# Performance work log

Measured on AMD Instinct MI355X. Metric: run time of the kernel, lower is better.

## Reference

```python
import jax, jax.numpy as jnp
import numpy as np

N, K, FEAT = 64, 32, 1024      # nodes, neighbors per node, input feature dim
C1, F1 = 4, 16                 # layer1: out_channels=4, out_features=hidden[0]/4=16
C2, F2 = 32, 1                 # layer2: out_channels=hidden[1]=32, out_features=1
NUM_CLASS = 10
BN_EPS = 1e-5


def _sgnroot(x):
    return jnp.sign(x) * jnp.sqrt(jnp.clip(jnp.abs(x), 1e-8))


def _feature_adjacency(x, nb):
    # x: (N,c,f), nb: (N,K,c,f) -> adj: (N,c,f,f)
    fadj = jnp.einsum('nca,nkcb->ncab', x, nb)          # sum over K neighbors
    fadj = fadj + jnp.swapaxes(fadj, -2, -1)
    s = _sgnroot(fadj)
    out = s / (jnp.abs(s).sum(axis=1, keepdims=True) + 1e-7)  # row-normalize over channel dim
    return jnp.where(jnp.isnan(out), 0.0, out)


def _layer(x, nb, W, c_out, f_out):
    # FeatTrans1d.forward: adjacency build + batched matmul + full-width conv (== dense contraction)
    n = x.shape[0]
    adj = _feature_adjacency(x, nb)                     # (N,c,f,f)
    xa = jnp.einsum('ncab,ncb->nca', adj, x)            # adj @ x
    x2 = jnp.einsum('ocf,ncf->no', W, xa).reshape(n, c_out, f_out)
    na = jnp.einsum('ncab,nkcb->nkca', adj, nb)         # per-node adj applied to its neighbors
    nb2 = jnp.einsum('ocf,nkcf->nko', W, na).reshape(n, -1, c_out, f_out)
    return x2, nb2


def _bn_softsign_x(x, w, b):
    # BatchNorm1d (training stats over batch+feature dims) + Softsign; x: (N,C,F)
    m = x.mean(axis=(0, 2), keepdims=True)
    v = x.var(axis=(0, 2), keepdims=True)
    y = (x - m) / jnp.sqrt(v + BN_EPS) * w[None, :, None] + b[None, :, None]
    return y / (1.0 + jnp.abs(y))


def _bn_softsign_nb(x, w, b):
    # each node's neighbor set is normalized independently (list comprehension in original); x: (N,K,C,F)
    m = x.mean(axis=(1, 3), keepdims=True)
    v = x.var(axis=(1, 3), keepdims=True)
    y = (x - m) / jnp.sqrt(v + BN_EPS) * w[None, None, :, None] + b[None, None, :, None]
    return y / (1.0 + jnp.abs(y))


def setup_inputs() -> dict:
    key = jax.random.key(0)
    ks = jax.random.split(key, 6)
    return {
        'x': jax.random.normal(ks[0], (N, 1, FEAT), jnp.float32),
        'neighbor': jax.random.normal(ks[1], (N, K, 1, FEAT), jnp.float32),
        'W1': jax.random.normal(ks[2], (C1 * F1, 1, FEAT), jnp.float32) * (1.0 / FEAT) ** 0.5,
        'W2': jax.random.normal(ks[3], (C2 * F2, C1, F1), jnp.float32) * (1.0 / (C1 * F1)) ** 0.5,
        'bn1_w': jnp.ones((C1,), jnp.float32),
        'bn1_b': jnp.zeros((C1,), jnp.float32),
        'bn2_w': jnp.ones((C2,), jnp.float32),
        'bn2_b': jnp.zeros((C2,), jnp.float32),
        'lin_w': jax.random.normal(ks[4], (NUM_CLASS, C2 * F2), jnp.float32) * (1.0 / (C2 * F2)) ** 0.5,
        'lin_b': jnp.zeros((NUM_CLASS,), jnp.float32),
    }


def reference(x, neighbor, W1, W2, bn1_w, bn1_b, bn2_w, bn2_b, lin_w, lin_b):
    x1, nb1 = _layer(x, neighbor, W1, C1, F1)           # (N,4,16), (N,K,4,16)
    x1 = _bn_softsign_x(x1, bn1_w, bn1_b)
    nb1 = _bn_softsign_nb(nb1, bn1_w, bn1_b)
    x2, _ = _layer(x1, nb1, W2, C2, F2)                 # (N,32,1)
    x2 = _bn_softsign_x(x2, bn2_w, bn2_b)
    return x2.reshape(x2.shape[0], -1) @ lin_w.T + lin_b  # (N,NUM_CLASS)
```

## Files before the change

kernel.cpp:

```cpp
#include <hip/hip_runtime.h>

typedef unsigned short u16;
typedef short short8 __attribute__((ext_vector_type(8)));
typedef float floatx4 __attribute__((ext_vector_type(4)));
typedef float floatx2 __attribute__((ext_vector_type(2)));
typedef unsigned int uintx4 __attribute__((ext_vector_type(4)));
typedef unsigned int uintx2 __attribute__((ext_vector_type(2)));
typedef u16 ushortx4 __attribute__((ext_vector_type(4)));

#define FEAT 1024
#define KNB  32

__device__ __forceinline__ u16 f2bf(float f) {
    unsigned u = __float_as_uint(f);
    u += 0x7fffu + ((u >> 16) & 1u);
    return (u16)(u >> 16);
}
__device__ __forceinline__ unsigned pack2bf(float a, float b) {
    return (unsigned)f2bf(a) | ((unsigned)f2bf(b) << 16);
}
__device__ __forceinline__ float softsign(float v) { return v / (1.f + fabsf(v)); }

union Frag { uintx4 q; unsigned d[4]; short8 v; };

__global__ __launch_bounds__(256, 2) void k2_main(
    const float* __restrict__ xg, const float* __restrict__ nbg,
    const float* __restrict__ w1g, float* __restrict__ pws)
{
    __shared__ float sS[FEAT];
    __shared__ float sX[FEAT];
    __shared__ u16  sY[34 * 1024];

    const int t = threadIdx.x;
    const int n = blockIdx.x >> 3;
    const int chunk = blockIdx.x & 7;
    const int chunkbase = chunk * 128;
    const int w = t >> 6;
    const int l = t & 63;
    const int m = l & 15;
    const int g = l >> 4;

    {
        ushortx4 z4 = {0, 0, 0, 0};
        *(ushortx4*)&sY[33 * 1024 + t * 4] = z4;
    }
    {
        floatx4 xv = *(const floatx4*)(xg + (size_t)n * FEAT + t * 4);
        *(floatx4*)&sX[t * 4] = xv;
        ushortx4 xb4 = {f2bf(xv[0]), f2bf(xv[1]), f2bf(xv[2]), f2bf(xv[3])};
        *(ushortx4*)&sY[t * 4] = xb4;
    }
    {
        const float* nbase = nbg + ((size_t)n * KNB) * FEAT + t * 4;
        floatx4 sacc = {0.f, 0.f, 0.f, 0.f};
        #pragma unroll 4
        for (int k = 0; k < KNB; ++k) {
            floatx4 v = *(const floatx4*)(nbase + (size_t)k * FEAT);
            sacc += v;
            int row = k + 1;
            int c16 = (t >> 1) ^ (row & 7);
            ushortx4 p4 = {f2bf(v[0]), f2bf(v[1]), f2bf(v[2]), f2bf(v[3])};
            *(ushortx4*)&sY[row * 1024 + c16 * 8 + (t & 1) * 4] = p4;
        }
        *(floatx4*)&sS[t * 4] = sacc;
    }

    const float xa0 = xg[(size_t)n * FEAT + chunkbase + w * 32 + m];
    const float xa1 = xg[(size_t)n * FEAT + chunkbase + w * 32 + 16 + m];
    __syncthreads();
    const float Sa0 = sS[chunkbase + w * 32 + m];
    const float Sa1 = sS[chunkbase + w * 32 + 16 + m];

    const u16* b2base = (m == 0) ? &sY[32 * 1024] : &sY[33 * 1024];
    const int sw = (m & 7);

    floatx4 acc[2][3];
    #pragma unroll
    for (int i = 0; i < 2; ++i)
        #pragma unroll
        for (int j = 0; j < 3; ++j) { floatx4 z = {0.f, 0.f, 0.f, 0.f}; acc[i][j] = z; }

    const floatx2 vxa0 = {xa0, xa0}, vxa1 = {xa1, xa1};
    const floatx2 vSa0 = {Sa0, Sa0}, vSa1 = {Sa1, Sa1};

    #pragma unroll 2
    for (int s = 0; s < 32; ++s) {
        const int bloc = s * 32 + g * 8;
        const int cidx = bloc >> 3;

        floatx4 xq0 = *(const floatx4*)&sX[bloc];
        floatx4 xq1 = *(const floatx4*)&sX[bloc + 4];
        floatx4 sq0 = *(const floatx4*)&sS[bloc];
        floatx4 sq1 = *(const floatx4*)&sS[bloc + 4];

        Frag af0, af1;
        #pragma unroll
        for (int p = 0; p < 4; ++p) {
            floatx2 xbp = (p < 2) ? ((p == 0) ? (floatx2){xq0[0], xq0[1]} : (floatx2){xq0[2], xq0[3]})
                                  : ((p == 2) ? (floatx2){xq1[0], xq1[1]} : (floatx2){xq1[2], xq1[3]});
            floatx2 sbp = (p < 2) ? ((p == 0) ? (floatx2){sq0[0], sq0[1]} : (floatx2){sq0[2], sq0[3]})
                                  : ((p == 2) ? (floatx2){sq1[0], sq1[1]} : (floatx2){sq1[2], sq1[3]});
            floatx2 u0 = xbp * vSa0 + sbp * vxa0;
            floatx2 u1 = xbp * vSa1 + sbp * vxa1;
            uintx2 b0b = __builtin_bit_cast(uintx2, u0);
            uintx2 b1b = __builtin_bit_cast(uintx2, u1);
            af0.d[p] = 0x3F803F80u | (b0b.y & 0x80000000u) | ((b0b.x >> 16) & 0x8000u);
            af1.d[p] = 0x3F803F80u | (b1b.y & 0x80000000u) | ((b1b.x >> 16) & 0x8000u);
        }

        Frag b0, b1, b2;
        b0.q = *(const uintx4*)&sY[ m       * 1024 + ((cidx ^ sw) << 3)];
        b1.q = *(const uintx4*)&sY[(16 + m) * 1024 + ((cidx ^ sw) << 3)];
        b2.q = *(const uintx4*)&b2base[cidx << 3];

        acc[0][0] = __builtin_amdgcn_mfma_f32_16x16x32_bf16(af0.v, b0.v, acc[0][0], 0, 0, 0);
        acc[0][1] = __builtin_amdgcn_mfma_f32_16x16x32_bf16(af0.v, b1.v, acc[0][1], 0, 0, 0);
        acc[0][2] = __builtin_amdgcn_mfma_f32_16x16x32_bf16(af0.v, b2.v, acc[0][2], 0, 0, 0);
        acc[1][0] = __builtin_amdgcn_mfma_f32_16x16x32_bf16(af1.v, b0.v, acc[1][0], 0, 0, 0);
        acc[1][1] = __builtin_amdgcn_mfma_f32_16x16x32_bf16(af1.v, b1.v, acc[1][1], 0, 0, 0);
        acc[1][2] = __builtin_amdgcn_mfma_f32_16x16x32_bf16(af1.v, b2.v, acc[1][2], 0, 0, 0);
    }
    __syncthreads();

    u16* sZ = sY;
    #pragma unroll
    for (int ti = 0; ti < 2; ++ti)
        #pragma unroll
        for (int jt = 0; jt < 3; ++jt) {
            int j = jt * 16 + m;
            int aloc = w * 32 + ti * 16 + g * 4;
            ushortx4 zz;
            zz.x = f2bf(acc[ti][jt][0]);
            zz.y = f2bf(acc[ti][jt][1]);
            zz.z = f2bf(acc[ti][jt][2]);
            zz.w = f2bf(acc[ti][jt][3]);
            *(ushortx4*)&sZ[j * 136 + aloc] = zz;
        }
    __syncthreads();

    floatx4 a2[3];
    #pragma unroll
    for (int j = 0; j < 3; ++j) { floatx4 z = {0.f, 0.f, 0.f, 0.f}; a2[j] = z; }
    #pragma unroll
    for (int kc = 0; kc < 4; ++kc) {
        const float* wsrc = w1g + (size_t)(w * 16 + m) * FEAT + chunkbase + kc * 32 + g * 8;
        floatx4 wf0 = *(const floatx4*)wsrc;
        floatx4 wf1 = *(const floatx4*)(wsrc + 4);
        Frag wb;
        wb.d[0] = pack2bf(wf0[0], wf0[1]);
        wb.d[1] = pack2bf(wf0[2], wf0[3]);
        wb.d[2] = pack2bf(wf1[0], wf1[1]);
        wb.d[3] = pack2bf(wf1[2], wf1[3]);
        #pragma unroll
        for (int jt = 0; jt < 3; ++jt) {
            Frag za;
            za.q = *(const uintx4*)&sZ[(jt * 16 + m) * 136 + kc * 32 + g * 8];
            a2[jt] = __builtin_amdgcn_mfma_f32_16x16x32_bf16(za.v, wb.v, a2[jt], 0, 0, 0);
        }
    }
    float* pbase = pws + (size_t)(n * 8 + chunk) * 33 * 64;
    #pragma unroll
    for (int jt = 0; jt < 3; ++jt)
        #pragma unroll
        for (int r = 0; r < 4; ++r) {
            int j = jt * 16 + g * 4 + r;
            if (j < 33) pbase[j * 64 + w * 16 + m] = a2[jt][r];
        }
}

__global__ __launch_bounds__(256, 1) void kB(
    const float* __restrict__ pws, const float* __restrict__ bn1w,
    const float* __restrict__ bn1b, const float* __restrict__ w2g,
    float* __restrict__ x22ws)
{
    __shared__ float sx2[64 * 64];
    __shared__ float snb[32 * 64];
    __shared__ float sx1[64], sS1[64], sadj[4 * 16 * 16], sxa[64];
    __shared__ float ssc[4], sbi[4], ssc2[4], sbi2[4];
    const int t = threadIdx.x;
    const int n = blockIdx.x;

    #pragma unroll
    for (int r = 0; r < 4; ++r) {
        int slot = t + r * 256;
        int nn = slot >> 4, oc = slot & 15;
        const float* p = pws + (size_t)nn * 16896 + oc * 4;
        floatx4 tmp[8];
        #pragma unroll
        for (int c = 0; c < 8; ++c) tmp[c] = *(const floatx4*)(p + c * 2112);
        floatx4 s01 = tmp[0] + tmp[1], s23 = tmp[2] + tmp[3];
        floatx4 s45 = tmp[4] + tmp[5], s67 = tmp[6] + tmp[7];
        *(floatx4*)&sx2[slot * 4] = (s01 + s23) + (s45 + s67);
    }
    #pragma unroll
    for (int r = 0; r < 2; ++r) {
        int slot = t + r * 256;
        int k = slot >> 4, oc = slot & 15;
        const float* p = pws + (size_t)n * 16896 + (1 + k) * 64 + oc * 4;
        floatx4 tmp[8];
        #pragma unroll
        for (int c = 0; c < 8; ++c) tmp[c] = *(const floatx4*)(p + c * 2112);
        floatx4 s01 = tmp[0] + tmp[1], s23 = tmp[2] + tmp[3];
        floatx4 s45 = tmp[4] + tmp[5], s67 = tmp[6] + tmp[7];
        *(floatx4*)&snb[slot * 4] = (s01 + s23) + (s45 + s67);
    }
    __syncthreads();
    {
        int cc = t >> 6, l2 = t & 63;
        float s = 0.f, s2 = 0.f;
        #pragma unroll
        for (int i = 0; i < 16; ++i) {
            int idx = l2 * 16 + i;
            int nn = idx >> 4, f = idx & 15;
            float v = sx2[nn * 64 + cc * 16 + f];
            s += v; s2 += v * v;
        }
        float s3 = 0.f, s4 = 0.f;
        #pragma unroll
        for (int i = 0; i < 8; ++i) {
            int idx = l2 * 8 + i;
            int k = idx >> 4, f = idx & 15;
            float v = snb[k * 64 + cc * 16 + f];
            s3 += v; s4 += v * v;
        }
        #pragma unroll
        for (int off = 32; off > 0; off >>= 1) {
            s  += __shfl_down(s, off);  s2 += __shfl_down(s2, off);
            s3 += __shfl_down(s3, off); s4 += __shfl_down(s4, off);
        }
        if (l2 == 0) {
            float wv = bn1w[cc], bv = bn1b[cc];
            float mean = s * (1.f / 1024.f);
            float var = s2 * (1.f / 1024.f) - mean * mean;
            float rs = rsqrtf(var + 1e-5f);
            ssc[cc] = rs * wv;
            sbi[cc] = bv - mean * rs * wv;
            float mean2 = s3 * (1.f / 512.f);
            float var2 = s4 * (1.f / 512.f) - mean2 * mean2;
            float rs2 = rsqrtf(var2 + 1e-5f);
            ssc2[cc] = rs2 * wv;
            sbi2[cc] = bv - mean2 * rs2 * wv;
        }
    }
    __syncthreads();
    if (t < 64) {
        int cc = t >> 4;
        sx1[t] = softsign(sx2[n * 64 + t] * ssc[cc] + sbi[cc]);
        float a = 0.f;
        for (int k = 0; k < KNB; ++k)
            a += softsign(snb[k * 64 + t] * ssc2[cc] + sbi2[cc]);
        sS1[t] = a;
    }
    __syncthreads();
    {
        int a = t >> 4, b = t & 15;
        float sc[4]; float den = 1e-7f;
        #pragma unroll
        for (int c = 0; c < 4; ++c) {
            float u = sx1[c * 16 + a] * sS1[c * 16 + b] + sx1[c * 16 + b] * sS1[c * 16 + a];
            float r = sqrtf(fmaxf(fabsf(u), 1e-8f));
            sc[c] = copysignf(r, u);
            den += r;
        }
        float inv = 1.f / den;
        #pragma unroll
        for (int c = 0; c < 4; ++c) sadj[(c * 16 + a) * 16 + b] = sc[c] * inv;
    }
    __syncthreads();
    if (t < 64) {
        int cc = t >> 4;
        float a = 0.f;
        #pragma unroll
        for (int b = 0; b < 16; ++b) a += sadj[t * 16 + b] * sx1[cc * 16 + b];
        sxa[t] = a;
    }
    __syncthreads();
    if (t < 32) {
        float a = 0.f;
        #pragma unroll
        for (int cf = 0; cf < 64; ++cf) a += w2g[t * 64 + cf] * sxa[cf];
        x22ws[n * 32 + t] = a;
    }
}

__global__ __launch_bounds__(256) void kC(
    const float* __restrict__ x22ws, const float* __restrict__ bn2w,
    const float* __restrict__ bn2b, const float* __restrict__ linw,
    const float* __restrict__ linb, float* __restrict__ outg)
{
    __shared__ float sy[64 * 32];
    __shared__ float ssc[32], sbi[32];
    __shared__ float sx[64 * 32];
    const int t = threadIdx.x;
    #pragma unroll
    for (int r = 0; r < 8; ++r) sx[t + r * 256] = x22ws[t + r * 256];
    __syncthreads();
    if (t < 32) {
        float s = 0.f, s2 = 0.f;
        for (int nn = 0; nn < 64; ++nn) {
            float v = sx[nn * 32 + t];
            s += v; s2 += v * v;
        }
        float mean = s * (1.f / 64.f);
        float var = s2 * (1.f / 64.f) - mean * mean;
        float rs = rsqrtf(var + 1e-5f);
        float wv = bn2w[t], bv = bn2b[t];
        ssc[t] = rs * wv;
        sbi[t] = bv - mean * rs * wv;
    }
    __syncthreads();
    #pragma unroll
    for (int r = 0; r < 8; ++r) {
        int idx = t + r * 256;
        int o = idx & 31;
        sy[idx] = softsign(sx[idx] * ssc[o] + sbi[o]);
    }
    __syncthreads();
    for (int r = 0; r < 3; ++r) {
        int idx = t + r * 256;
        if (idx < 640) {
            int nn = idx / 10, cls = idx % 10;
            float a = linb[cls];
            #pragma unroll
            for (int o = 0; o < 32; ++o) a += sy[nn * 32 + o] * linw[cls * 32 + o];
            outg[idx] = a;
        }
    }
}

extern "C" void kernel_launch(void* const* d_in, const int* in_sizes, int n_in,
                              void* d_out, int out_size, void* d_ws, size_t ws_size,
                              hipStream_t stream) {
    (void)in_sizes; (void)n_in; (void)out_size; (void)ws_size;
    const float* xg   = (const float*)d_in[0];
    const float* nbg  = (const float*)d_in[1];
    const float* w1g  = (const float*)d_in[2];
    const float* w2g  = (const float*)d_in[3];
    const float* bn1w = (const float*)d_in[4];
    const float* bn1b = (const float*)d_in[5];
    const float* bn2w = (const float*)d_in[6];
    const float* bn2b = (const float*)d_in[7];
    const float* linw = (const float*)d_in[8];
    const float* linb = (const float*)d_in[9];

    float* pws   = (float*)d_ws;
    float* x22ws = pws + (size_t)64 * 8 * 33 * 64;
    float* outg  = (float*)d_out;

    k2_main<<<dim3(512), dim3(256), 0, stream>>>(xg, nbg, w1g, pws);
    kB<<<dim3(64), dim3(256), 0, stream>>>(pws, bn1w, bn1b, w2g, x22ws);
    kC<<<dim3(1), dim3(256), 0, stream>>>(x22ws, bn2w, bn2b, linw, linb, outg);
}
```

Baseline: 107.6 us.

## Halve k2_main grid with wider chunks and fuse final kernel via last-block counter

Each k2_main block now covers a 256-feature chunk with four row tiles per wave instead of two. This halves the grid to 256 blocks, so the per-node neighbor loading and bf16 staging are done half as often, and kB reduces four partials instead of eight. The single-block kC kernel is folded into kB: an atomic counter, reset in k2_main, picks the last finishing block to run BN2, softsign and the linear layer, removing one launch. The cost is more registers per thread (12 accumulators), fewer blocks to fill the GPU, and reliance on atomic ordering.

```diff
diff --git a/kernel.cpp b/kernel.cpp
--- a/kernel.cpp
+++ b/kernel.cpp
@@ -10,6 +10,7 @@
 
 #define FEAT 1024
 #define KNB  32
+#define ZSTR 268
 
 __device__ __forceinline__ u16 f2bf(float f) {
     unsigned u = __float_as_uint(f);
@@ -23,22 +24,26 @@
 
 union Frag { uintx4 q; unsigned d[4]; short8 v; };
 
-__global__ __launch_bounds__(256, 2) void k2_main(
+__global__ __launch_bounds__(256) void k2_main(
     const float* __restrict__ xg, const float* __restrict__ nbg,
-    const float* __restrict__ w1g, float* __restrict__ pws)
+    const float* __restrict__ w1g, float* __restrict__ pws,
+    unsigned* __restrict__ cntws)
 {
     __shared__ float sS[FEAT];
     __shared__ float sX[FEAT];
     __shared__ u16  sY[34 * 1024];
 
     const int t = threadIdx.x;
-    const int n = blockIdx.x >> 3;
-    const int chunk = blockIdx.x & 7;
-    const int chunkbase = chunk * 128;
+    const int n = blockIdx.x >> 2;
+    const int chunk = blockIdx.x & 3;
+    const int chunkbase = chunk * 256;
     const int w = t >> 6;
     const int l = t & 63;
     const int m = l & 15;
     const int g = l >> 4;
+
+    if (blockIdx.x == 0 && t == 0)
+        __hip_atomic_store(cntws, 0u, __ATOMIC_RELEASE, __HIP_MEMORY_SCOPE_AGENT);
 
     {
         ushortx4 z4 = {0, 0, 0, 0};
@@ -65,23 +70,24 @@
         *(floatx4*)&sS[t * 4] = sacc;
     }
 
-    const float xa0 = xg[(size_t)n * FEAT + chunkbase + w * 32 + m];
-    const float xa1 = xg[(size_t)n * FEAT + chunkbase + w * 32 + 16 + m];
-    __syncthreads();
-    const float Sa0 = sS[chunkbase + w * 32 + m];
-    const float Sa1 = sS[chunkbase + w * 32 + 16 + m];
+    float xa[4];
+    #pragma unroll
+    for (int ti = 0; ti < 4; ++ti)
+        xa[ti] = xg[(size_t)n * FEAT + chunkbase + w * 64 + ti * 16 + m];
+    __syncthreads();
+    float Sa[4];
+    #pragma unroll
+    for (int ti = 0; ti < 4; ++ti)
+        Sa[ti] = sS[chunkbase + w * 64 + ti * 16 + m];
 
     const u16* b2base = (m == 0) ? &sY[32 * 1024] : &sY[33 * 1024];
     const int sw = (m & 7);
 
-    floatx4 acc[2][3];
-    #pragma unroll
-    for (int i = 0; i < 2; ++i)
+    floatx4 acc[4][3];
+    #pragma unroll
+    for (int i = 0; i < 4; ++i)
         #pragma unroll
         for (int j = 0; j < 3; ++j) { floatx4 z = {0.f, 0.f, 0.f, 0.f}; acc[i][j] = z; }
-
-    const floatx2 vxa0 = {xa0, xa0}, vxa1 = {xa1, xa1};
-    const floatx2 vSa0 = {Sa0, Sa0}, vSa1 = {Sa1, Sa1};
 
     #pragma unroll 2
     for (int s = 0; s < 32; ++s) {
@@ -93,19 +99,21 @@
         floatx4 sq0 = *(const floatx4*)&sS[bloc];
         floatx4 sq1 = *(const floatx4*)&sS[bloc + 4];
 
-        Frag af0, af1;
+        Frag af[4];
         #pragma unroll
         for (int p = 0; p < 4; ++p) {
             floatx2 xbp = (p < 2) ? ((p == 0) ? (floatx2){xq0[0], xq0[1]} : (floatx2){xq0[2], xq0[3]})
                                   : ((p == 2) ? (floatx2){xq1[0], xq1[1]} : (floatx2){xq1[2], xq1[3]});
             floatx2 sbp = (p < 2) ? ((p == 0) ? (floatx2){sq0[0], sq0[1]} : (floatx2){sq0[2], sq0[3]})
                                   : ((p == 2) ? (floatx2){sq1[0], sq1[1]} : (floatx2){sq1[2], sq1[3]});
-            floatx2 u0 = xbp * vSa0 + sbp * vxa0;
-            floatx2 u1 = xbp * vSa1 + sbp * vxa1;
-            uintx2 b0b = __builtin_bit_cast(uintx2, u0);
-            uintx2 b1b = __builtin_bit_cast(uintx2, u1);
-            af0.d[p] = 0x3F803F80u | (b0b.y & 0x80000000u) | ((b0b.x >> 16) & 0x8000u);
-            af1.d[p] = 0x3F803F80u | (b1b.y & 0x80000000u) | ((b1b.x >> 16) & 0x8000u);
+            #pragma unroll
+            for (int ti = 0; ti < 4; ++ti) {
+                floatx2 vsa = {Sa[ti], Sa[ti]};
+                floatx2 vxa = {xa[ti], xa[ti]};
+                floatx2 u = xbp * vsa + sbp * vxa;
+                uintx2 ub = __builtin_bit_cast(uintx2, u);
+                af[ti].d[p] = 0x3F803F80u | (ub.y & 0x80000000u) | ((ub.x >> 16) & 0x8000u);
+            }
         }
 
         Frag b0, b1, b2;
@@ -113,28 +121,28 @@
         b1.q = *(const uintx4*)&sY[(16 + m) * 1024 + ((cidx ^ sw) << 3)];
         b2.q = *(const uintx4*)&b2base[cidx << 3];
 
-        acc[0][0] = __builtin_amdgcn_mfma_f32_16x16x32_bf16(af0.v, b0.v, acc[0][0], 0, 0, 0);
-        acc[0][1] = __builtin_amdgcn_mfma_f32_16x16x32_bf16(af0.v, b1.v, acc[0][1], 0, 0, 0);
-        acc[0][2] = __builtin_amdgcn_mfma_f32_16x16x32_bf16(af0.v, b2.v, acc[0][2], 0, 0, 0);
-        acc[1][0] = __builtin_amdgcn_mfma_f32_16x16x32_bf16(af1.v, b0.v, acc[1][0], 0, 0, 0);
-        acc[1][1] = __builtin_amdgcn_mfma_f32_16x16x32_bf16(af1.v, b1.v, acc[1][1], 0, 0, 0);
-        acc[1][2] = __builtin_amdgcn_mfma_f32_16x16x32_bf16(af1.v, b2.v, acc[1][2], 0, 0, 0);
+        #pragma unroll
+        for (int ti = 0; ti < 4; ++ti) {
+            acc[ti][0] = __builtin_amdgcn_mfma_f32_16x16x32_bf16(af[ti].v, b0.v, acc[ti][0], 0, 0, 0);
+            acc[ti][1] = __builtin_amdgcn_mfma_f32_16x16x32_bf16(af[ti].v, b1.v, acc[ti][1], 0, 0, 0);
+            acc[ti][2] = __builtin_amdgcn_mfma_f32_16x16x32_bf16(af[ti].v, b2.v, acc[ti][2], 0, 0, 0);
+        }
     }
     __syncthreads();
 
     u16* sZ = sY;
     #pragma unroll
-    for (int ti = 0; ti < 2; ++ti)
+    for (int ti = 0; ti < 4; ++ti)
         #pragma unroll
         for (int jt = 0; jt < 3; ++jt) {
             int j = jt * 16 + m;
-            int aloc = w * 32 + ti * 16 + g * 4;
+            int aloc = w * 64 + ti * 16 + g * 4;
             ushortx4 zz;
             zz.x = f2bf(acc[ti][jt][0]);
             zz.y = f2bf(acc[ti][jt][1]);
             zz.z = f2bf(acc[ti][jt][2]);
             zz.w = f2bf(acc[ti][jt][3]);
-            *(ushortx4*)&sZ[j * 136 + aloc] = zz;
+            *(ushortx4*)&sZ[j * ZSTR + aloc] = zz;
         }
     __syncthreads();
 
@@ -142,7 +150,7 @@
     #pragma unroll
     for (int j = 0; j < 3; ++j) { floatx4 z = {0.f, 0.f, 0.f, 0.f}; a2[j] = z; }
     #pragma unroll
-    for (int kc = 0; kc < 4; ++kc) {
+    for (int kc = 0; kc < 8; ++kc) {
         const float* wsrc = w1g + (size_t)(w * 16 + m) * FEAT + chunkbase + kc * 32 + g * 8;
         floatx4 wf0 = *(const floatx4*)wsrc;
         floatx4 wf1 = *(const floatx4*)(wsrc + 4);
@@ -154,11 +162,11 @@
         #pragma unroll
         for (int jt = 0; jt < 3; ++jt) {
             Frag za;
-            za.q = *(const uintx4*)&sZ[(jt * 16 + m) * 136 + kc * 32 + g * 8];
+            za.q = *(const uintx4*)&sZ[(jt * 16 + m) * ZSTR + kc * 32 + g * 8];
             a2[jt] = __builtin_amdgcn_mfma_f32_16x16x32_bf16(za.v, wb.v, a2[jt], 0, 0, 0);
         }
     }
-    float* pbase = pws + (size_t)(n * 8 + chunk) * 33 * 64;
+    float* pbase = pws + (size_t)(n * 4 + chunk) * 33 * 64;
     #pragma unroll
     for (int jt = 0; jt < 3; ++jt)
         #pragma unroll
@@ -171,12 +179,17 @@
 __global__ __launch_bounds__(256, 1) void kB(
     const float* __restrict__ pws, const float* __restrict__ bn1w,
     const float* __restrict__ bn1b, const float* __restrict__ w2g,
-    float* __restrict__ x22ws)
+    const float* __restrict__ bn2w, const float* __restrict__ bn2b,
+    const float* __restrict__ linw, const float* __restrict__ linb,
+    float* __restrict__ x22ws, float* __restrict__ outg,
+    unsigned* __restrict__ cntws)
 {
     __shared__ float sx2[64 * 64];
     __shared__ float snb[32 * 64];
     __shared__ float sx1[64], sS1[64], sadj[4 * 16 * 16], sxa[64];
     __shared__ float ssc[4], sbi[4], ssc2[4], sbi2[4];
+    __shared__ float sscB[32], sbiB[32];
+    __shared__ unsigned slast;
     const int t = threadIdx.x;
     const int n = blockIdx.x;
 
@@ -184,25 +197,21 @@
     for (int r = 0; r < 4; ++r) {
         int slot = t + r * 256;
         int nn = slot >> 4, oc = slot & 15;
-        const float* p = pws + (size_t)nn * 16896 + oc * 4;
-        floatx4 tmp[8];
-        #pragma unroll
-        for (int c = 0; c < 8; ++c) tmp[c] = *(const floatx4*)(p + c * 2112);
-        floatx4 s01 = tmp[0] + tmp[1], s23 = tmp[2] + tmp[3];
-        floatx4 s45 = tmp[4] + tmp[5], s67 = tmp[6] + tmp[7];
-        *(floatx4*)&sx2[slot * 4] = (s01 + s23) + (s45 + s67);
+        const float* p = pws + (size_t)nn * 8448 + oc * 4;
+        floatx4 tmp[4];
+        #pragma unroll
+        for (int c = 0; c < 4; ++c) tmp[c] = *(const floatx4*)(p + c * 2112);
+        *(floatx4*)&sx2[slot * 4] = (tmp[0] + tmp[1]) + (tmp[2] + tmp[3]);
     }
     #pragma unroll
     for (int r = 0; r < 2; ++r) {
         int slot = t + r * 256;
         int k = slot >> 4, oc = slot & 15;
-        const float* p = pws + (size_t)n * 16896 + (1 + k) * 64 + oc * 4;
-        floatx4 tmp[8];
-        #pragma unroll
-        for (int c = 0; c < 8; ++c) tmp[c] = *(const floatx4*)(p + c * 2112);
-        floatx4 s01 = tmp[0] + tmp[1], s23 = tmp[2] + tmp[3];
-        floatx4 s45 = tmp[4] + tmp[5], s67 = tmp[6] + tmp[7];
-        *(floatx4*)&snb[slot * 4] = (s01 + s23) + (s45 + s67);
+        const float* p = pws + (size_t)n * 8448 + (1 + k) * 64 + oc * 4;
+        floatx4 tmp[4];
+        #pragma unroll
+        for (int c = 0; c < 4; ++c) tmp[c] = *(const floatx4*)(p + c * 2112);
+        *(floatx4*)&snb[slot * 4] = (tmp[0] + tmp[1]) + (tmp[2] + tmp[3]);
     }
     __syncthreads();
     {
@@ -279,41 +288,45 @@
         float a = 0.f;
         #pragma unroll
         for (int cf = 0; cf < 64; ++cf) a += w2g[t * 64 + cf] * sxa[cf];
-        x22ws[n * 32 + t] = a;
-    }
-}
-
-__global__ __launch_bounds__(256) void kC(
-    const float* __restrict__ x22ws, const float* __restrict__ bn2w,
-    const float* __restrict__ bn2b, const float* __restrict__ linw,
-    const float* __restrict__ linb, float* __restrict__ outg)
-{
-    __shared__ float sy[64 * 32];
-    __shared__ float ssc[32], sbi[32];
-    __shared__ float sx[64 * 32];
-    const int t = threadIdx.x;
-    #pragma unroll
-    for (int r = 0; r < 8; ++r) sx[t + r * 256] = x22ws[t + r * 256];
+        __hip_atomic_store(&x22ws[n * 32 + t], a, __ATOMIC_RELEASE, __HIP_MEMORY_SCOPE_AGENT);
+    }
+    __syncthreads();
+    if (t == 0) {
+        unsigned old = __hip_atomic_fetch_add(cntws, 1u, __ATOMIC_ACQ_REL,
+                                              __HIP_MEMORY_SCOPE_AGENT);
+        slast = (old == 63u) ? 1u : 0u;
+    }
+    __syncthreads();
+    if (!slast) return;
+
+    float* sall = sx2;
+    float* sy2  = sx2 + 2048;
+    #pragma unroll
+    for (int r = 0; r < 8; ++r) {
+        int idx = t + r * 256;
+        sall[idx] = __hip_atomic_load(&x22ws[idx], __ATOMIC_ACQUIRE,
+                                      __HIP_MEMORY_SCOPE_AGENT);
+    }
     __syncthreads();
     if (t < 32) {
         float s = 0.f, s2 = 0.f;
         for (int nn = 0; nn < 64; ++nn) {
-            float v = sx[nn * 32 + t];
+            float v = sall[nn * 32 + t];
             s += v; s2 += v * v;
         }
         float mean = s * (1.f / 64.f);
         float var = s2 * (1.f / 64.f) - mean * mean;
         float rs = rsqrtf(var + 1e-5f);
         float wv = bn2w[t], bv = bn2b[t];
-        ssc[t] = rs * wv;
-        sbi[t] = bv - mean * rs * wv;
+        sscB[t] = rs * wv;
+        sbiB[t] = bv - mean * rs * wv;
     }
     __syncthreads();
     #pragma unroll
     for (int r = 0; r < 8; ++r) {
         int idx = t + r * 256;
         int o = idx & 31;
-        sy[idx] = softsign(sx[idx] * ssc[o] + sbi[o]);
+        sy2[idx] = softsign(sall[idx] * sscB[o] + sbiB[o]);
     }
     __syncthreads();
     for (int r = 0; r < 3; ++r) {
@@ -322,7 +335,7 @@
             int nn = idx / 10, cls = idx % 10;
             float a = linb[cls];
             #pragma unroll
-            for (int o = 0; o < 32; ++o) a += sy[nn * 32 + o] * linw[cls * 32 + o];
+            for (int o = 0; o < 32; ++o) a += sy2[nn * 32 + o] * linw[cls * 32 + o];
             outg[idx] = a;
         }
     }
@@ -343,11 +356,13 @@
     const float* linw = (const float*)d_in[8];
     const float* linb = (const float*)d_in[9];
 
-    float* pws   = (float*)d_ws;
-    float* x22ws = pws + (size_t)64 * 8 * 33 * 64;
-    float* outg  = (float*)d_out;
-
-    k2_main<<<dim3(512), dim3(256), 0, stream>>>(xg, nbg, w1g, pws);
-    kB<<<dim3(64), dim3(256), 0, stream>>>(pws, bn1w, bn1b, w2g, x22ws);
-    kC<<<dim3(1), dim3(256), 0, stream>>>(x22ws, bn2w, bn2b, linw, linb, outg);
-}
+    float* pws      = (float*)d_ws;
+    float* x22ws    = pws + (size_t)64 * 4 * 33 * 64;
+    unsigned* cntws = (unsigned*)(x22ws + 64 * 32);
+    float* outg     = (float*)d_out;
+
+    k2_main<<<dim3(256), dim3(256), 0, stream>>>(xg, nbg, w1g, pws, cntws);
+    kB<<<dim3(64), dim3(256), 0, stream>>>(pws, bn1w, bn1b, w2g,
+                                           bn2w, bn2b, linw, linb,
+                                           x22ws, outg, cntws);
+}
```

Measured after the change: 109.1 us. No clear change (+1.4%).

## Fuse final BN/linear kernel into kB via last-block atomic counter

Applied to the files above, without the earlier changes.

Removes the third kernel launch by having each kB block atomically increment a counter after writing its layer-2 outputs. The last block to finish then runs the batch-norm, softsign and linear classifier. The counter is reset by the first kernel. The sign-packing of MFMA A-fragments now uses a byte-permute builtin instead of shifts and masks. This saves one launch and its gap at the cost of atomics and a serialized tail in one block.

```diff
diff --git a/kernel.cpp b/kernel.cpp
--- a/kernel.cpp
+++ b/kernel.cpp
@@ -21,11 +21,21 @@
 }
 __device__ __forceinline__ float softsign(float v) { return v / (1.f + fabsf(v)); }
 
+__device__ __forceinline__ unsigned signpack(unsigned blo, unsigned bhi) {
+#if __has_builtin(__builtin_amdgcn_perm)
+    unsigned p = __builtin_amdgcn_perm(bhi, blo, 0x07080308u);
+    return (p & 0x80008000u) | 0x3F803F80u;
+#else
+    return 0x3F803F80u | (bhi & 0x80000000u) | ((blo >> 16) & 0x8000u);
+#endif
+}
+
 union Frag { uintx4 q; unsigned d[4]; short8 v; };
 
 __global__ __launch_bounds__(256, 2) void k2_main(
     const float* __restrict__ xg, const float* __restrict__ nbg,
-    const float* __restrict__ w1g, float* __restrict__ pws)
+    const float* __restrict__ w1g, float* __restrict__ pws,
+    unsigned* __restrict__ cntws)
 {
     __shared__ float sS[FEAT];
     __shared__ float sX[FEAT];
@@ -39,6 +49,9 @@
     const int l = t & 63;
     const int m = l & 15;
     const int g = l >> 4;
+
+    if (blockIdx.x == 0 && t == 0)
+        __hip_atomic_store(cntws, 0u, __ATOMIC_RELEASE, __HIP_MEMORY_SCOPE_AGENT);
 
     {
         ushortx4 z4 = {0, 0, 0, 0};
@@ -104,8 +117,8 @@
             floatx2 u1 = xbp * vSa1 + sbp * vxa1;
             uintx2 b0b = __builtin_bit_cast(uintx2, u0);
             uintx2 b1b = __builtin_bit_cast(uintx2, u1);
-            af0.d[p] = 0x3F803F80u | (b0b.y & 0x80000000u) | ((b0b.x >> 16) & 0x8000u);
-            af1.d[p] = 0x3F803F80u | (b1b.y & 0x80000000u) | ((b1b.x >> 16) & 0x8000u);
+            af0.d[p] = signpack(b0b.x, b0b.y);
+            af1.d[p] = signpack(b1b.x, b1b.y);
         }
 
         Frag b0, b1, b2;
@@ -171,12 +184,17 @@
 __global__ __launch_bounds__(256, 1) void kB(
     const float* __restrict__ pws, const float* __restrict__ bn1w,
     const float* __restrict__ bn1b, const float* __restrict__ w2g,
-    float* __restrict__ x22ws)
+    const float* __restrict__ bn2w, const float* __restrict__ bn2b,
+    const float* __restrict__ linw, const float* __restrict__ linb,
+    float* __restrict__ x22ws, float* __restrict__ outg,
+    unsigned* __restrict__ cntws)
 {
     __shared__ float sx2[64 * 64];
     __shared__ float snb[32 * 64];
     __shared__ float sx1[64], sS1[64], sadj[4 * 16 * 16], sxa[64];
     __shared__ float ssc[4], sbi[4], ssc2[4], sbi2[4];
+    __shared__ float sscB[32], sbiB[32];
+    __shared__ unsigned slast;
     const int t = threadIdx.x;
     const int n = blockIdx.x;
 
@@ -279,41 +297,45 @@
         float a = 0.f;
         #pragma unroll
         for (int cf = 0; cf < 64; ++cf) a += w2g[t * 64 + cf] * sxa[cf];
-        x22ws[n * 32 + t] = a;
-    }
-}
-
-__global__ __launch_bounds__(256) void kC(
-    const float* __restrict__ x22ws, const float* __restrict__ bn2w,
-    const float* __restrict__ bn2b, const float* __restrict__ linw,
-    const float* __restrict__ linb, float* __restrict__ outg)
-{
-    __shared__ float sy[64 * 32];
-    __shared__ float ssc[32], sbi[32];
-    __shared__ float sx[64 * 32];
-    const int t = threadIdx.x;
-    #pragma unroll
-    for (int r = 0; r < 8; ++r) sx[t + r * 256] = x22ws[t + r * 256];
+        __hip_atomic_store(&x22ws[n * 32 + t], a, __ATOMIC_RELEASE, __HIP_MEMORY_SCOPE_AGENT);
+    }
+    __syncthreads();
+    if (t == 0) {
+        unsigned old = __hip_atomic_fetch_add(cntws, 1u, __ATOMIC_ACQ_REL,
+                                              __HIP_MEMORY_SCOPE_AGENT);
+        slast = (old == 63u) ? 1u : 0u;
+    }
+    __syncthreads();
+    if (!slast) return;
+
+    float* sall = sx2;
+    float* sy2  = sx2 + 2048;
+    #pragma unroll
+    for (int r = 0; r < 8; ++r) {
+        int idx = t + r * 256;
+        sall[idx] = __hip_atomic_load(&x22ws[idx], __ATOMIC_ACQUIRE,
+                                      __HIP_MEMORY_SCOPE_AGENT);
+    }
     __syncthreads();
     if (t < 32) {
         float s = 0.f, s2 = 0.f;
         for (int nn = 0; nn < 64; ++nn) {
-            float v = sx[nn * 32 + t];
+            float v = sall[nn * 32 + t];
             s += v; s2 += v * v;
         }
         float mean = s * (1.f / 64.f);
         float var = s2 * (1.f / 64.f) - mean * mean;
         float rs = rsqrtf(var + 1e-5f);
         float wv = bn2w[t], bv = bn2b[t];
-        ssc[t] = rs * wv;
-        sbi[t] = bv - mean * rs * wv;
+        sscB[t] = rs * wv;
+        sbiB[t] = bv - mean * rs * wv;
     }
     __syncthreads();
     #pragma unroll
     for (int r = 0; r < 8; ++r) {
         int idx = t + r * 256;
         int o = idx & 31;
-        sy[idx] = softsign(sx[idx] * ssc[o] + sbi[o]);
+        sy2[idx] = softsign(sall[idx] * sscB[o] + sbiB[o]);
     }
     __syncthreads();
     for (int r = 0; r < 3; ++r) {
@@ -322,7 +344,7 @@
             int nn = idx / 10, cls = idx % 10;
             float a = linb[cls];
             #pragma unroll
-            for (int o = 0; o < 32; ++o) a += sy[nn * 32 + o] * linw[cls * 32 + o];
+            for (int o = 0; o < 32; ++o) a += sy2[nn * 32 + o] * linw[cls * 32 + o];
             outg[idx] = a;
         }
     }
@@ -343,11 +365,13 @@
     const float* linw = (const float*)d_in[8];
     const float* linb = (const float*)d_in[9];
 
-    float* pws   = (float*)d_ws;
-    float* x22ws = pws + (size_t)64 * 8 * 33 * 64;
-    float* outg  = (float*)d_out;
-
-    k2_main<<<dim3(512), dim3(256), 0, stream>>>(xg, nbg, w1g, pws);
-    kB<<<dim3(64), dim3(256), 0, stream>>>(pws, bn1w, bn1b, w2g, x22ws);
-    kC<<<dim3(1), dim3(256), 0, stream>>>(x22ws, bn2w, bn2b, linw, linb, outg);
-}
+    float* pws      = (float*)d_ws;
+    float* x22ws    = pws + (size_t)64 * 8 * 33 * 64;
+    unsigned* cntws = (unsigned*)(x22ws + 64 * 32);
+    float* outg     = (float*)d_out;
+
+    k2_main<<<dim3(512), dim3(256), 0, stream>>>(xg, nbg, w1g, pws, cntws);
+    kB<<<dim3(64), dim3(256), 0, stream>>>(pws, bn1w, bn1b, w2g,
+                                           bn2w, bn2b, linw, linb,
+                                           x22ws, outg, cntws);
+}
```

Result: slower. 113.4 us (+5.4%).
